# Optimization experiments

Measured on AMD Instinct MI355X. Metric: run time of the kernel, lower is better.

The kernel has to match this reference:

```python
import jax, jax.numpy as jnp
import numpy as np
from jax import lax

SCOPE = 63
DECAY = 0.05
MAX_STEPS = 20
CONV_THRESH = 0.001
STD = 2.0


def mexican_hat(scope, std):
    # standard Ricker wavelet, matching weight_initialization.mexican_hat(scope, std=2)
    x = np.linspace(-(scope // 2), scope // 2, scope).astype(np.float32)
    norm = 2.0 / (np.sqrt(3.0 * std) * np.pi ** 0.25)
    w = norm * (1.0 - (x / std) ** 2) * np.exp(-x ** 2 / (2.0 * std ** 2))
    return jnp.asarray(w, dtype=jnp.float32)


def setup_inputs() -> dict:
    key = jax.random.key(0)
    activations = jax.random.normal(key, (16, 512, 32, 32), dtype=jnp.float32)
    w = mexican_hat(SCOPE, STD)
    # Conv3d weight layout OIDHW = [1,1,scope,1,1]; W_rec is a deepcopy of W_in
    w_in = w.reshape(1, 1, SCOPE, 1, 1)
    w_rec = w.reshape(1, 1, SCOPE, 1, 1)
    return {"activations": activations, "w_in": w_in, "w_rec": w_rec}


def _conv_channel(x5, w):
    # x5: [B,1,C,H,W]; conv along C only ('same' padding since scope is odd)
    p = SCOPE // 2
    return lax.conv_general_dilated(
        x5, w, window_strides=(1, 1, 1),
        padding=[(p, p), (0, 0), (0, 0)],
        dimension_numbers=("NCDHW", "OIDHW", "NCDHW"))


def reference(activations, w_in, w_rec):
    x5 = activations[:, None]                      # [B,1,C,H,W]
    inhib_in = _conv_channel(x5, w_in)             # [B,1,C,H,W]

    def step(carry, _):
        state, done = carry
        rec = _conv_channel(state, w_rec)
        phi = (inhib_in + rec) * 0.5
        cand = (1.0 - DECAY) * state + DECAY * phi
        diff = jnp.mean((cand - state) ** 2)       # MSE between successive states
        new_state = jnp.where(done, state, cand)   # freeze after convergence (early stop)
        done = done | (diff <= CONV_THRESH)
        return (new_state, done), None

    (final, _), _ = lax.scan(step, (inhib_in, jnp.array(False)), None, length=MAX_STEPS)
    return final[:, 0]                             # [B,C,H,W]
```

## Files before the change

kernel.cpp:

```cpp
#include <hip/hip_runtime.h>

#define DD       512
#define Q4       256
#define DSEG     8
#define HALO     31
#define NWIN     70
#define WZN      77
#define SCOPE    63
#define MAXSTEPS 20
#define NELEMD   8388608.0
#define NSLOT    8
#define NTHREADS 256
#define NBLOCKS  1024

__device__ __forceinline__ unsigned short f2bf(float f) {
    unsigned int b = __float_as_uint(f);
    b += 0x7FFFu + ((b >> 16) & 1u);
    return (unsigned short)(b >> 16);
}
__device__ __forceinline__ float bf2f(unsigned short u) {
    return __uint_as_float(((unsigned int)u) << 16);
}

__global__ void build_kernel(const float* __restrict__ w_in,
                             const float* __restrict__ w_rec,
                             float* __restrict__ wzin,
                             float* __restrict__ wzrec,
                             double* __restrict__ dacc,
                             int* __restrict__ done)
{
    const int t = threadIdx.x;
    if (t < WZN) {
        const int k = t - (DSEG - 1);
        const bool v = (k >= 0 && k < SCOPE);
        wzin[t]  = v ? w_in[k]  : 0.f;
        wzrec[t] = v ? w_rec[k] : 0.f;
    }
    if (t < (MAXSTEPS + 1) * NSLOT)
        dacc[t * 8] = (t < NSLOT) ? 1e30 : 0.0;
    if (t == 0) *done = 0;
}

__device__ __forceinline__ void fir8(const float4* __restrict__ src,
                                     const float* __restrict__ wz,
                                     const int rowbase, const int d0, const int q,
                                     float4* __restrict__ acc)
{
    #pragma unroll
    for (int r = 0; r < DSEG; ++r) acc[r] = make_float4(0.f, 0.f, 0.f, 0.f);
    #pragma unroll 7
    for (int j = 0; j < NWIN; ++j) {
        const int d   = d0 + j - HALO;
        const int dcl = min(max(d, 0), DD - 1);
        float4 x = src[((rowbase + dcl) << 8) + q];
        if ((unsigned)d >= DD) x = make_float4(0.f, 0.f, 0.f, 0.f);
        #pragma unroll
        for (int r = 0; r < DSEG; ++r) {
            const float wk = wz[j - r + (DSEG - 1)];
            acc[r].x = fmaf(wk, x.x, acc[r].x);
            acc[r].y = fmaf(wk, x.y, acc[r].y);
            acc[r].z = fmaf(wk, x.z, acc[r].z);
            acc[r].w = fmaf(wk, x.w, acc[r].w);
        }
    }
}

__device__ __forceinline__ void decode_block(int bid, int& rowbase, int& d0) {
    const int nb = (bid & 7) * (NBLOCKS / 8) + (bid >> 3);
    rowbase = (nb >> 6) * DD;
    d0      = (nb & 63) * DSEG;
}

__global__ __launch_bounds__(NTHREADS, 2)
void step0_kernel(const float4* __restrict__ act,
                  float4* __restrict__ b0,
                  ushort4* __restrict__ ib,
                  const float* __restrict__ wzin)
{
    int rowbase, d0; decode_block(blockIdx.x, rowbase, d0);
    const int q = threadIdx.x;

    float4 acc[DSEG];
    fir8(act, wzin, rowbase, d0, q, acc);
    #pragma unroll
    for (int r = 0; r < DSEG; ++r) {
        const int idx = ((rowbase + d0 + r) << 8) + q;
        b0[idx] = acc[r];
        ushort4 u;
        u.x = f2bf(acc[r].x); u.y = f2bf(acc[r].y);
        u.z = f2bf(acc[r].z); u.w = f2bf(acc[r].w);
        ib[idx] = u;
    }
}

__global__ __launch_bounds__(NTHREADS, 2)
void step_kernel(const float4* __restrict__ src,
                 float4* __restrict__ dst,
                 const ushort4* __restrict__ ib,
                 const float* __restrict__ wzrec,
                 double* __restrict__ dacc,
                 int* __restrict__ done,
                 const int s)
{
    if (__hip_atomic_load(done, __ATOMIC_RELAXED, __HIP_MEMORY_SCOPE_AGENT)) return;

    double prev = 0.0;
    #pragma unroll
    for (int sl = 0; sl < NSLOT; ++sl)
        prev += dacc[((s - 1) * NSLOT + sl) * 8];
    if ((float)(prev / NELEMD) <= 0.001f) {
        if (threadIdx.x == 0)
            __hip_atomic_store(done, 1, __ATOMIC_RELAXED, __HIP_MEMORY_SCOPE_AGENT);
        return;
    }

    int rowbase, d0; decode_block(blockIdx.x, rowbase, d0);
    const int q = threadIdx.x;

    float4 acc[DSEG];
    fir8(src, wzrec, rowbase, d0, q, acc);

    double lsum = 0.0;
    #pragma unroll
    for (int r = 0; r < DSEG; ++r) {
        const int idx = ((rowbase + d0 + r) << 8) + q;
        const float4  sv = src[idx];
        const ushort4 u  = ib[idx];
        float4 c;
        c.x = 0.95f * sv.x + 0.05f * ((bf2f(u.x) + acc[r].x) * 0.5f);
        c.y = 0.95f * sv.y + 0.05f * ((bf2f(u.y) + acc[r].y) * 0.5f);
        c.z = 0.95f * sv.z + 0.05f * ((bf2f(u.z) + acc[r].z) * 0.5f);
        c.w = 0.95f * sv.w + 0.05f * ((bf2f(u.w) + acc[r].w) * 0.5f);
        const float dx = c.x - sv.x, dy = c.y - sv.y;
        const float dz = c.z - sv.z, dw = c.w - sv.w;
        lsum += (double)(dx * dx) + (double)(dy * dy)
              + (double)(dz * dz) + (double)(dw * dw);
        dst[idx] = c;
    }

    #pragma unroll
    for (int off = 32; off > 0; off >>= 1)
        lsum += __shfl_down(lsum, off, 64);
    __shared__ double wred[NTHREADS / 64];
    if ((threadIdx.x & 63) == 0) wred[threadIdx.x >> 6] = lsum;
    __syncthreads();
    if (threadIdx.x == 0)
        atomicAdd(&dacc[(s * NSLOT + (blockIdx.x & 7)) * 8],
                  wred[0] + wred[1] + wred[2] + wred[3]);
}

__global__ __launch_bounds__(NTHREADS, 2)
void final_kernel(const float4* __restrict__ b0,
                  float4* __restrict__ out,
                  const double* __restrict__ dacc)
{
    int T = MAXSTEPS;
    for (int t = 1; t <= MAXSTEPS; ++t) {
        double v = 0.0;
        #pragma unroll
        for (int sl = 0; sl < NSLOT; ++sl) v += dacc[(t * NSLOT + sl) * 8];
        if ((float)(v / NELEMD) <= 0.001f) { T = t; break; }
    }
    if (T & 1) return;

    int rowbase, d0; decode_block(blockIdx.x, rowbase, d0);
    const int q = threadIdx.x;
    #pragma unroll
    for (int r = 0; r < DSEG; ++r) {
        const int idx = ((rowbase + d0 + r) << 8) + q;
        out[idx] = b0[idx];
    }
}

extern "C" void kernel_launch(void* const* d_in, const int* in_sizes, int n_in,
                              void* d_out, int out_size, void* d_ws, size_t ws_size,
                              hipStream_t stream) {
    const float* act   = (const float*)d_in[0];
    const float* w_in  = (const float*)d_in[1];
    const float* w_rec = (const float*)d_in[2];

    char* ws = (char*)d_ws;
    float4*  b0    = (float4*)ws;
    ushort4* ib    = (ushort4*)(ws + (40u << 20));
    double*  dacc  = (double*)(ws + (60u << 20));
    float*   wzin  = (float*)(ws + (60u << 20) + (16u << 10));
    float*   wzrec = wzin + 128;
    int*     done  = (int*)(wzrec + 128);
    float4*  b1    = (float4*)d_out;

    build_kernel<<<1, NTHREADS, 0, stream>>>(w_in, w_rec, wzin, wzrec, dacc, done);
    step0_kernel<<<NBLOCKS, NTHREADS, 0, stream>>>((const float4*)act, b0, ib, wzin);
    for (int s = 1; s <= MAXSTEPS; ++s) {
        const float4* src = (s & 1) ? (const float4*)b0 : (const float4*)b1;
        float4*       dst = (s & 1) ? b1 : b0;
        step_kernel<<<NBLOCKS, NTHREADS, 0, stream>>>(src, dst, ib, wzrec, dacc, done, s);
    }
    final_kernel<<<NBLOCKS, NTHREADS, 0, stream>>>(b0, b1, dacc);
}
```

Baseline: 189.0 us.

## Stage channel window tiles in LDS and compute FIR from shared memory

Each block now loads a 126-row by 32-column float4 window of the source into shared memory and runs the 63-tap channel convolution from LDS. Before, every thread read its 70-row window straight from global memory. Blocks now cover 64 output rows with 512 threads, each thread computing 4 rows, which lets neighbouring threads reuse the halo through LDS and cuts redundant global and L2 traffic. The step's old state is also read from LDS, and the final copy uses a flat index. The cost is about 64KB of LDS per block, which may limit occupancy, plus an extra barrier.

After: 178.4 us. 1.06x faster.

```diff
diff --git a/kernel.cpp b/kernel.cpp
--- a/kernel.cpp
+++ b/kernel.cpp
@@ -2,15 +2,18 @@
 
 #define DD       512
 #define Q4       256
-#define DSEG     8
+#define DSEG     4
+#define ROWB     64
+#define COLB     32
 #define HALO     31
-#define NWIN     70
-#define WZN      77
+#define WROWS    126
+#define NWIN     66
+#define WZN      69
 #define SCOPE    63
 #define MAXSTEPS 20
 #define NELEMD   8388608.0
 #define NSLOT    8
-#define NTHREADS 256
+#define NTHREADS 512
 #define NBLOCKS  1024
 
 __device__ __forceinline__ unsigned short f2bf(float f) {
@@ -41,19 +44,44 @@
     if (t == 0) *done = 0;
 }
 
-__device__ __forceinline__ void fir8(const float4* __restrict__ src,
+__device__ __forceinline__ void decode_block(int bid, int& rowbase, int& d0, int& colg) {
+    const int nb = (bid & 7) * (NBLOCKS / 8) + (bid >> 3);
+    rowbase = (nb >> 6) * DD;
+    d0      = ((nb >> 3) & 7) * ROWB;
+    colg    = (nb & 7) * COLB;
+}
+
+__device__ __forceinline__ void stage(const float4* __restrict__ src,
+                                      float4 (*S)[COLB],
+                                      const int rowbase, const int d0, const int colg)
+{
+    const int c = threadIdx.x & (COLB - 1);
+    const int g = threadIdx.x >> 5;
+    #pragma unroll
+    for (int k = 0; k < 8; ++k) {
+        const int wrow = g + 16 * k;
+        if (wrow < WROWS) {
+            const int d = d0 - HALO + wrow;
+            float4 v = make_float4(0.f, 0.f, 0.f, 0.f);
+            if ((unsigned)d < DD)
+                v = src[(rowbase + d) * Q4 + colg + c];
+            S[wrow][c] = v;
+        }
+    }
+}
+
+__device__ __forceinline__ void fir4(const float4 (*S)[COLB],
                                      const float* __restrict__ wz,
-                                     const int rowbase, const int d0, const int q,
                                      float4* __restrict__ acc)
 {
+    const int c = threadIdx.x & (COLB - 1);
+    const int g = threadIdx.x >> 5;
+    const int l0 = 4 * g;
     #pragma unroll
     for (int r = 0; r < DSEG; ++r) acc[r] = make_float4(0.f, 0.f, 0.f, 0.f);
-    #pragma unroll 7
+    #pragma unroll 6
     for (int j = 0; j < NWIN; ++j) {
-        const int d   = d0 + j - HALO;
-        const int dcl = min(max(d, 0), DD - 1);
-        float4 x = src[((rowbase + dcl) << 8) + q];
-        if ((unsigned)d >= DD) x = make_float4(0.f, 0.f, 0.f, 0.f);
+        const float4 x = S[l0 + j][c];
         #pragma unroll
         for (int r = 0; r < DSEG; ++r) {
             const float wk = wz[j - r + (DSEG - 1)];
@@ -65,26 +93,26 @@
     }
 }
 
-__device__ __forceinline__ void decode_block(int bid, int& rowbase, int& d0) {
-    const int nb = (bid & 7) * (NBLOCKS / 8) + (bid >> 3);
-    rowbase = (nb >> 6) * DD;
-    d0      = (nb & 63) * DSEG;
-}
-
 __global__ __launch_bounds__(NTHREADS, 2)
 void step0_kernel(const float4* __restrict__ act,
                   float4* __restrict__ b0,
                   ushort4* __restrict__ ib,
                   const float* __restrict__ wzin)
 {
-    int rowbase, d0; decode_block(blockIdx.x, rowbase, d0);
-    const int q = threadIdx.x;
+    __shared__ float4 S[WROWS][COLB];
+    int rowbase, d0, colg; decode_block(blockIdx.x, rowbase, d0, colg);
+    const int c = threadIdx.x & (COLB - 1);
+    const int g = threadIdx.x >> 5;
+
+    stage(act, S, rowbase, d0, colg);
+    __syncthreads();
 
     float4 acc[DSEG];
-    fir8(act, wzin, rowbase, d0, q, acc);
+    fir4(S, wzin, acc);
+
     #pragma unroll
     for (int r = 0; r < DSEG; ++r) {
-        const int idx = ((rowbase + d0 + r) << 8) + q;
+        const int idx = (rowbase + d0 + 4 * g + r) * Q4 + colg + c;
         b0[idx] = acc[r];
         ushort4 u;
         u.x = f2bf(acc[r].x); u.y = f2bf(acc[r].y);
@@ -114,28 +142,34 @@
         return;
     }
 
-    int rowbase, d0; decode_block(blockIdx.x, rowbase, d0);
-    const int q = threadIdx.x;
+    __shared__ float4 S[WROWS][COLB];
+    int rowbase, d0, colg; decode_block(blockIdx.x, rowbase, d0, colg);
+    const int c = threadIdx.x & (COLB - 1);
+    const int g = threadIdx.x >> 5;
+
+    stage(src, S, rowbase, d0, colg);
+    __syncthreads();
 
     float4 acc[DSEG];
-    fir8(src, wzrec, rowbase, d0, q, acc);
+    fir4(S, wzrec, acc);
 
     double lsum = 0.0;
     #pragma unroll
     for (int r = 0; r < DSEG; ++r) {
-        const int idx = ((rowbase + d0 + r) << 8) + q;
-        const float4  sv = src[idx];
+        const int row = d0 + 4 * g + r;
+        const int idx = (rowbase + row) * Q4 + colg + c;
+        const float4  sv = S[4 * g + HALO + r][c];
         const ushort4 u  = ib[idx];
-        float4 c;
-        c.x = 0.95f * sv.x + 0.05f * ((bf2f(u.x) + acc[r].x) * 0.5f);
-        c.y = 0.95f * sv.y + 0.05f * ((bf2f(u.y) + acc[r].y) * 0.5f);
-        c.z = 0.95f * sv.z + 0.05f * ((bf2f(u.z) + acc[r].z) * 0.5f);
-        c.w = 0.95f * sv.w + 0.05f * ((bf2f(u.w) + acc[r].w) * 0.5f);
-        const float dx = c.x - sv.x, dy = c.y - sv.y;
-        const float dz = c.z - sv.z, dw = c.w - sv.w;
+        float4 cv;
+        cv.x = 0.95f * sv.x + 0.05f * ((bf2f(u.x) + acc[r].x) * 0.5f);
+        cv.y = 0.95f * sv.y + 0.05f * ((bf2f(u.y) + acc[r].y) * 0.5f);
+        cv.z = 0.95f * sv.z + 0.05f * ((bf2f(u.z) + acc[r].z) * 0.5f);
+        cv.w = 0.95f * sv.w + 0.05f * ((bf2f(u.w) + acc[r].w) * 0.5f);
+        const float dx = cv.x - sv.x, dy = cv.y - sv.y;
+        const float dz = cv.z - sv.z, dw = cv.w - sv.w;
         lsum += (double)(dx * dx) + (double)(dy * dy)
               + (double)(dz * dz) + (double)(dw * dw);
-        dst[idx] = c;
+        dst[idx] = cv;
     }
 
     #pragma unroll
@@ -144,9 +178,12 @@
     __shared__ double wred[NTHREADS / 64];
     if ((threadIdx.x & 63) == 0) wred[threadIdx.x >> 6] = lsum;
     __syncthreads();
-    if (threadIdx.x == 0)
-        atomicAdd(&dacc[(s * NSLOT + (blockIdx.x & 7)) * 8],
-                  wred[0] + wred[1] + wred[2] + wred[3]);
+    if (threadIdx.x == 0) {
+        double bs = 0.0;
+        #pragma unroll
+        for (int q = 0; q < NTHREADS / 64; ++q) bs += wred[q];
+        atomicAdd(&dacc[(s * NSLOT + (blockIdx.x & 7)) * 8], bs);
+    }
 }
 
 __global__ __launch_bounds__(NTHREADS, 2)
@@ -163,11 +200,10 @@
     }
     if (T & 1) return;
 
-    int rowbase, d0; decode_block(blockIdx.x, rowbase, d0);
-    const int q = threadIdx.x;
-    #pragma unroll
-    for (int r = 0; r < DSEG; ++r) {
-        const int idx = ((rowbase + d0 + r) << 8) + q;
+    const int gid = blockIdx.x * NTHREADS + threadIdx.x;
+    #pragma unroll
+    for (int r = 0; r < 4; ++r) {
+        const int idx = gid + r * (NBLOCKS * NTHREADS);
         out[idx] = b0[idx];
     }
 }
@@ -188,7 +224,7 @@
     int*     done  = (int*)(wzrec + 128);
     float4*  b1    = (float4*)d_out;
 
-    build_kernel<<<1, NTHREADS, 0, stream>>>(w_in, w_rec, wzin, wzrec, dacc, done);
+    build_kernel<<<1, 256, 0, stream>>>(w_in, w_rec, wzin, wzrec, dacc, done);
     step0_kernel<<<NBLOCKS, NTHREADS, 0, stream>>>((const float4*)act, b0, ib, wzin);
     for (int s = 1; s <= MAXSTEPS; ++s) {
         const float4* src = (s & 1) ? (const float4*)b0 : (const float4*)b1;
```
